# Performance work log

Hardware: AMD Instinct MI355X
Metric: run time of the kernel (lower is better)

The kernel has to match this reference:

```python
import math
import jax, jax.numpy as jnp
import numpy as np

N_HEAD = 32
HEAD_DIM = 64
ROTARY_DIM = 32
ROTARY_BASE = 10000.0


def _rope(u, cos, sin):
    # u: [B, S, H, head_dim]; cos/sin: [S, ROTARY_DIM//2]
    u_rot = u[..., :ROTARY_DIM].astype(jnp.float32)
    u1, u2 = jnp.split(u_rot, 2, axis=-1)          # [B,S,H,rot/2] each
    c = cos[None, :, None, :]
    s = sin[None, :, None, :]
    r = jnp.concatenate([u1 * c - u2 * s, u1 * s + u2 * c], axis=-1).astype(u.dtype)
    return jnp.concatenate([r, u[..., ROTARY_DIM:]], axis=-1)


def setup_inputs() -> dict:
    key = jax.random.key(0)
    ks = jax.random.split(key, 5)
    B, S, D = 2, 2048, 2048
    std = 1.0 / math.sqrt(D)
    x = jax.random.normal(ks[0], (B, S, D), dtype=jnp.float32)
    Wqkv = jax.random.normal(ks[1], (D, 3 * D), dtype=jnp.float32) * std
    b_qkv = jax.random.normal(ks[2], (3 * D,), dtype=jnp.float32) * 0.01
    Wout = jax.random.normal(ks[3], (D, D), dtype=jnp.float32) * std
    b_out = jax.random.normal(ks[4], (D,), dtype=jnp.float32) * 0.01
    return {"x": x, "Wqkv": Wqkv, "b_qkv": b_qkv, "Wout": Wout, "b_out": b_out}


def reference(x, Wqkv, b_qkv, Wout, b_out):
    B, S, D = x.shape
    H, hd = N_HEAD, HEAD_DIM
    # QKV projection -> [B, S, 3, H, hd]
    qkv = (x @ Wqkv + b_qkv).reshape(B, S, 3, H, hd)
    # Rotary cos/sin cache (fp32 position indices, as in the module)
    inv_freq = 1.0 / (ROTARY_BASE ** (jnp.arange(0, ROTARY_DIM, 2, dtype=jnp.float32) / ROTARY_DIM))
    t = jnp.arange(S, dtype=jnp.float32)
    freqs = jnp.outer(t, inv_freq)                 # [S, ROTARY_DIM//2]
    cos, sin = jnp.cos(freqs), jnp.sin(freqs)
    q = _rope(qkv[:, :, 0], cos, sin)
    k = _rope(qkv[:, :, 1], cos, sin)
    v = qkv[:, :, 2]
    scale = 1.0 / math.sqrt(hd)
    scores = jnp.einsum('bthd,bshd->bhts', q, k * scale)   # [B,H,S,S]
    rows = jnp.arange(S)[:, None]
    cols = jnp.arange(S)[None, :]
    causal_mask = cols > rows                      # seqlen_k == seqlen_q here
    scores = jnp.where(causal_mask[None, None], jnp.asarray(-10000.0, scores.dtype), scores)
    attn = jax.nn.softmax(scores, axis=-1)         # dropout p=0.0
    out = jnp.einsum('bhts,bshd->bthd', attn, v).reshape(B, S, D)
    return out @ Wout + b_out
```

## Files before the change

kernel.cpp:

```cpp
#include <hip/hip_runtime.h>
#include <stdint.h>
#include <math.h>

#define DEV static __device__ __forceinline__

typedef __attribute__((ext_vector_type(8))) short bf16x8;
typedef __attribute__((ext_vector_type(4))) float f32x4;
typedef __attribute__((ext_vector_type(8))) unsigned short u16x8;
typedef __attribute__((ext_vector_type(4))) unsigned short u16x4;
typedef __attribute__((ext_vector_type(2))) unsigned int u32x2;

enum { B_ = 2, S_ = 2048, D_ = 2048, H_ = 32, HD_ = 64, N3_ = 6144, M_ = 4096 };

DEV unsigned short f2bf(float f) {
  unsigned u = __float_as_uint(f);
  u += 0x7FFFu + ((u >> 16) & 1u);
  return (unsigned short)(u >> 16);
}
DEV float bf2f(unsigned short s) { return __uint_as_float(((unsigned)s) << 16); }

DEV void load16(const void* g, void* l) {
  __builtin_amdgcn_global_load_lds((const __attribute__((address_space(1))) void*)g,
                                   (__attribute__((address_space(3))) void*)l,
                                   16, 0, 0);
}

DEV f32x4 mfma16(bf16x8 a, bf16x8 b, f32x4 c) {
  return __builtin_amdgcn_mfma_f32_16x16x32_bf16(a, b, c, 0, 0, 0);
}

__global__ __launch_bounds__(256) void cvt_bf16(const float* __restrict__ in,
                                                unsigned short* __restrict__ out, int n) {
  int i = blockIdx.x * 256 + threadIdx.x;
  if (i * 8 >= n) return;
  const float4* in4 = (const float4*)in;
  float4 a = in4[i * 2 + 0];
  float4 b = in4[i * 2 + 1];
  u16x8 o;
  o[0] = f2bf(a.x); o[1] = f2bf(a.y); o[2] = f2bf(a.z); o[3] = f2bf(a.w);
  o[4] = f2bf(b.x); o[5] = f2bf(b.y); o[6] = f2bf(b.z); o[7] = f2bf(b.w);
  *(u16x8*)(out + (size_t)i * 8) = o;
}

__global__ __launch_bounds__(256) void transpose_bf16(const float* __restrict__ W,
                                                      unsigned short* __restrict__ Wt,
                                                      int Kg, int Ng) {
  __shared__ float tile[32][33];
  const int tn = blockIdx.x, tk = blockIdx.y;
  const int t = threadIdx.x;
  const int r = t >> 3, c4 = (t & 7) * 4;
  float4 v = *(const float4*)(W + (size_t)(tk * 32 + r) * Ng + tn * 32 + c4);
  tile[r][c4 + 0] = v.x; tile[r][c4 + 1] = v.y;
  tile[r][c4 + 2] = v.z; tile[r][c4 + 3] = v.w;
  __syncthreads();
  u16x4 o;
  o[0] = f2bf(tile[c4 + 0][r]);
  o[1] = f2bf(tile[c4 + 1][r]);
  o[2] = f2bf(tile[c4 + 2][r]);
  o[3] = f2bf(tile[c4 + 3][r]);
  *(u16x4*)(Wt + (size_t)(tn * 32 + r) * Kg + tk * 32 + c4) = o;
}

template <int MODE>
__global__ __launch_bounds__(512, 2) void gemm256(const unsigned short* __restrict__ A,
                                                  const unsigned short* __restrict__ BT,
                                                  const float* __restrict__ bias,
                                                  void* __restrict__ Cout,
                                                  int Mg, int Ng, int Kg) {
  __shared__ __align__(16) char lds[131072];
  const int tid = threadIdx.x;
  const int lane = tid & 63, w = tid >> 6;
  const int g = (lane >> 4) & 3, l16 = lane & 15;
  const int wm = w >> 2, wn = w & 3;

  const int wg = (blockIdx.x & 7) * (gridDim.x >> 3) + (blockIdx.x >> 3);
  const int nTM = Mg >> 8;
  const int tm = wg % nTM, tn = wg / nTM;
  const int rb = tm * 256, cb = tn * 256;
  const int NT = Kg >> 6;

  const int offA = (wm * 128 + l16) * 128;
  const int offB = 32768 + (wn * 64 + l16) * 128;
  const int su0 = ((0 + g) ^ (l16 & 7)) * 16;
  const int su1 = ((4 + g) ^ (l16 & 7)) * 16;

  const unsigned short* sA[4]; const unsigned short* sB[4];
  int dA[4], dB[4];
#pragma unroll
  for (int c = 0; c < 4; ++c) {
    int Uc = c * 512 + tid, row = Uc >> 3, u = (Uc & 7) ^ (row & 7);
    sA[c] = A + (size_t)(rb + row) * Kg + u * 8;
    sB[c] = BT + (size_t)(cb + row) * Kg + u * 8;
    dA[c] = Uc * 16; dB[c] = 32768 + Uc * 16;
  }

  auto STAGE = [&](int t) {
    char* _b = (char*)lds + ((t & 1) << 16);
#pragma unroll
    for (int c = 0; c < 4; ++c) {
      load16(sA[c] + (size_t)t * 64, _b + dA[c]);
      load16(sB[c] + (size_t)t * 64, _b + dB[c]);
    }
  };

  STAGE(0); STAGE(1);
  asm volatile("s_waitcnt vmcnt(8)" ::: "memory");
  __builtin_amdgcn_s_barrier();

  f32x4 acc[8][4] = {};

  for (int t = 0; t < NT; ++t) {
    const char* bs = (const char*)lds + ((t & 1) << 16);
    bf16x8 a[4][2], b[4][2];
#pragma unroll
    for (int mf = 0; mf < 4; ++mf) {
      a[mf][0] = *(const bf16x8*)(bs + offA + mf * 2048 + su0);
      a[mf][1] = *(const bf16x8*)(bs + offA + mf * 2048 + su1);
    }
#pragma unroll
    for (int nf = 0; nf < 4; ++nf) {
      b[nf][0] = *(const bf16x8*)(bs + offB + nf * 2048 + su0);
      b[nf][1] = *(const bf16x8*)(bs + offB + nf * 2048 + su1);
    }
#pragma unroll
    for (int mf = 0; mf < 4; ++mf)
#pragma unroll
      for (int nf = 0; nf < 4; ++nf)
#pragma unroll
        for (int kh = 0; kh < 2; ++kh)
          acc[mf][nf] = mfma16(a[mf][kh], b[nf][kh], acc[mf][nf]);
#pragma unroll
    for (int mf = 0; mf < 4; ++mf) {
      a[mf][0] = *(const bf16x8*)(bs + offA + (mf + 4) * 2048 + su0);
      a[mf][1] = *(const bf16x8*)(bs + offA + (mf + 4) * 2048 + su1);
    }
#pragma unroll
    for (int mf = 0; mf < 4; ++mf)
#pragma unroll
      for (int nf = 0; nf < 4; ++nf)
#pragma unroll
        for (int kh = 0; kh < 2; ++kh)
          acc[mf + 4][nf] = mfma16(a[mf][kh], b[nf][kh], acc[mf + 4][nf]);

    asm volatile("s_waitcnt lgkmcnt(0)" ::: "memory");
    __builtin_amdgcn_s_barrier();
    if (t + 2 < NT) {
      STAGE(t + 2);
      asm volatile("s_waitcnt vmcnt(8)" ::: "memory");
    } else {
      asm volatile("s_waitcnt vmcnt(0)" ::: "memory");
    }
    __builtin_amdgcn_s_barrier();
  }

  const int crow0 = rb + wm * 128 + g * 4;
  const int ccol0 = cb + wn * 64 + l16;
  float bv[4];
#pragma unroll
  for (int nf = 0; nf < 4; ++nf) bv[nf] = bias[ccol0 + nf * 16];

  if (MODE == 1) {
    unsigned short* O = (unsigned short*)Cout;
    const bool dorot = (cb + wn * 64) < 4096;
    const float inv = exp2f(-(float)l16 * 0.83048202372184056f);
#pragma unroll
    for (int mf = 0; mf < 8; ++mf)
#pragma unroll
      for (int r = 0; r < 4; ++r) {
        int row = crow0 + mf * 16 + r;
        float v0 = acc[mf][0][r] + bv[0];
        float v1 = acc[mf][1][r] + bv[1];
        float v2 = acc[mf][2][r] + bv[2];
        float v3 = acc[mf][3][r] + bv[3];
        if (dorot) {
          float sn, cs;
          sincosf((float)(row & (S_ - 1)) * inv, &sn, &cs);
          float t0 = v0 * cs - v1 * sn;
          v1 = v0 * sn + v1 * cs;
          v0 = t0;
        }
        unsigned short* p = O + (size_t)row * Ng + ccol0;
        p[0] = f2bf(v0); p[16] = f2bf(v1); p[32] = f2bf(v2); p[48] = f2bf(v3);
      }
  } else {
    float* O = (float*)Cout;
#pragma unroll
    for (int mf = 0; mf < 8; ++mf)
#pragma unroll
      for (int r = 0; r < 4; ++r) {
        int row = crow0 + mf * 16 + r;
        float* p = O + (size_t)row * Ng + ccol0;
        p[0] = acc[mf][0][r] + bv[0];
        p[16] = acc[mf][1][r] + bv[1];
        p[32] = acc[mf][2][r] + bv[2];
        p[48] = acc[mf][3][r] + bv[3];
      }
  }
}

DEV int xsw(int row) { return (row ^ (row >> 2)) & 3; }

template <int OUT_BF16>
__global__ __launch_bounds__(256) void gemm_bt(const unsigned short* __restrict__ A,
                                               const unsigned short* __restrict__ BT,
                                               const float* __restrict__ bias,
                                               void* __restrict__ Cout,
                                               int Mg, int Ng, int Kg) {
  __shared__ __align__(16) unsigned short lA[128 * 32];
  __shared__ __align__(16) unsigned short lB[128 * 32];
  const int tid = threadIdx.x;
  const int lane = tid & 63, wv = tid >> 6;
  const int g = lane >> 4, l16 = lane & 15;
  const int wr = wv >> 1, wc = wv & 1;
  const int rb = blockIdx.x * 128, cb = blockIdx.y * 128;

  f32x4 acc[4][4] = {};

  for (int k0 = 0; k0 < Kg; k0 += 32) {
    __syncthreads();
#pragma unroll
    for (int c = 0; c < 2; ++c) {
      int p = c * 256 + tid;
      int row = p >> 2;
      int k8l = (p & 3) ^ xsw(row);
      load16(A + (size_t)(rb + row) * Kg + k0 + 8 * k8l, (char*)lA + p * 16);
      load16(BT + (size_t)(cb + row) * Kg + k0 + 8 * k8l, (char*)lB + p * 16);
    }
    __syncthreads();
    bf16x8 af[4], bfr[4];
#pragma unroll
    for (int m = 0; m < 4; ++m) {
      int row = wr * 64 + m * 16 + l16;
      af[m] = *(const bf16x8*)((const char*)lA + (size_t)(row * 4 + (g ^ xsw(row))) * 16);
    }
#pragma unroll
    for (int n = 0; n < 4; ++n) {
      int row = wc * 64 + n * 16 + l16;
      bfr[n] = *(const bf16x8*)((const char*)lB + (size_t)(row * 4 + (g ^ xsw(row))) * 16);
    }
#pragma unroll
    for (int m = 0; m < 4; ++m)
#pragma unroll
      for (int n = 0; n < 4; ++n)
        acc[m][n] = mfma16(af[m], bfr[n], acc[m][n]);
  }

#pragma unroll
  for (int m = 0; m < 4; ++m)
#pragma unroll
    for (int n = 0; n < 4; ++n)
#pragma unroll
      for (int r = 0; r < 4; ++r) {
        int row = rb + wr * 64 + m * 16 + g * 4 + r;
        int col = cb + wc * 64 + n * 16 + l16;
        float v = acc[m][n][r] + bias[col];
        if (OUT_BF16)
          ((unsigned short*)Cout)[(size_t)row * Ng + col] = f2bf(v);
        else
          ((float*)Cout)[(size_t)row * Ng + col] = v;
      }
}

__global__ __launch_bounds__(256) void vtrans(const unsigned short* __restrict__ qkv,
                                              unsigned short* __restrict__ vt) {
  __shared__ unsigned short tile[64][72];
  const int s0 = blockIdx.x * 64;
  const int bh = blockIdx.y;
  const int b = bh >> 5, h = bh & 31;
  const int t = threadIdx.x;
#pragma unroll
  for (int c = 0; c < 2; ++c) {
    int sl = (c * 256 + t) >> 3, d8 = t & 7;
    u16x8 v = *(const u16x8*)(qkv + (size_t)(b * S_ + s0 + sl) * N3_ + 4096 + h * 64 + d8 * 8);
    *(u16x8*)(&tile[sl][d8 * 8]) = v;
  }
  __syncthreads();
#pragma unroll
  for (int c = 0; c < 2; ++c) {
    int dl = (c * 256 + t) >> 3, s8 = t & 7;
    u16x8 o;
#pragma unroll
    for (int j = 0; j < 8; ++j) o[j] = tile[s8 * 8 + j][dl];
    *(u16x8*)(vt + (size_t)(bh * 64 + dl) * S_ + s0 + s8 * 8) = o;
  }
}

DEV void stage_kv(const unsigned short* __restrict__ qkv,
                  const unsigned short* __restrict__ vt,
                  unsigned char* lds, int bS, int bh64, int hoff, int kvb, int buf, int tid) {
#pragma unroll
  for (int c = 0; c < 2; ++c) {
    int p = c * 256 + tid;
    int row = p >> 3, k8 = (p & 7) ^ (row & 7);
    load16(qkv + (size_t)(bS + kvb + row) * N3_ + 2048 + hoff + 8 * k8,
           lds + buf * 8192 + p * 16);
    load16(vt + (size_t)(bh64 + row) * S_ + kvb + 8 * k8,
           lds + 16384 + buf * 8192 + p * 16);
  }
}

__global__ __launch_bounds__(256, 3) void attn_kernel(const unsigned short* __restrict__ qkv,
                                                      const unsigned short* __restrict__ vt,
                                                      unsigned short* __restrict__ ao) {
  __shared__ __align__(16) unsigned char lds[49152];
  const int tid = threadIdx.x;
  const int lane = tid & 63, wv = tid >> 6;
  const int g = lane >> 4, l16 = lane & 15;
  const int bid = blockIdx.x;
  const int qi = 15 - (bid >> 6);
  const int t6 = bid & 63;
  const int bh = ((t6 & 7) << 3) | (t6 >> 3);
  const int b = bh >> 5, h = bh & 31;
  const int qbase = qi * 128;
  const int srow0 = qbase + wv * 32;
  const int bS = b * S_, bh64 = bh * 64, hoff = h * 64;

  bf16x8 qf[2][2];
#pragma unroll
  for (int m = 0; m < 2; ++m)
#pragma unroll
    for (int kt = 0; kt < 2; ++kt)
      qf[m][kt] = *(const bf16x8*)(qkv + (size_t)(bS + srow0 + m * 16 + l16) * N3_ +
                                   hoff + kt * 32 + g * 8);

  float mrun[2] = {-INFINITY, -INFINITY}, lrun[2] = {0.f, 0.f};
  f32x4 o[2][4] = {};
  unsigned char* pw = lds + 32768 + wv * 4096;

  const int nkv = (qbase + 128) >> 6;
  stage_kv(qkv, vt, lds, bS, bh64, hoff, 0, 0, tid);
  __syncthreads();

  for (int kb = 0; kb < nkv; ++kb) {
    const int cur = kb & 1;
    if (kb + 1 < nkv) stage_kv(qkv, vt, lds, bS, bh64, hoff, (kb + 1) << 6, cur ^ 1, tid);
    const int kvb = kb << 6;
    if (kvb <= srow0 + 31) {
      const unsigned char* kbuf = lds + cur * 8192;
      const unsigned char* vbuf = lds + 16384 + cur * 8192;

      f32x4 sc[2][4];
#pragma unroll
      for (int n = 0; n < 4; ++n) {
        int row = n * 16 + l16;
        bf16x8 kf0 = *(const bf16x8*)(kbuf + (row * 8 + ((g + 0) ^ (row & 7))) * 16);
        bf16x8 kf1 = *(const bf16x8*)(kbuf + (row * 8 + ((g + 4) ^ (row & 7))) * 16);
#pragma unroll
        for (int m = 0; m < 2; ++m) {
          f32x4 z = {};
          z = mfma16(kf0, qf[m][0], z);
          z = mfma16(kf1, qf[m][1], z);
          sc[m][n] = z;
        }
      }

      const bool boundary = (kvb + 63 > srow0);
#pragma unroll
      for (int m = 0; m < 2; ++m) {
        const int qrow = srow0 + m * 16 + l16;
        if (boundary) {
#pragma unroll
          for (int n = 0; n < 4; ++n)
#pragma unroll
            for (int r = 0; r < 4; ++r) {
              int k = kvb + n * 16 + g * 4 + r;
              if (k > qrow) sc[m][n][r] = -INFINITY;
            }
        }
        float mx = fmaxf(fmaxf(sc[m][0][0], sc[m][0][1]), fmaxf(sc[m][0][2], sc[m][0][3]));
#pragma unroll
        for (int n = 1; n < 4; ++n)
          mx = fmaxf(mx, fmaxf(fmaxf(sc[m][n][0], sc[m][n][1]), fmaxf(sc[m][n][2], sc[m][n][3])));
        mx = fmaxf(mx, __shfl_xor(mx, 16));
        mx = fmaxf(mx, __shfl_xor(mx, 32));
        float pm = mx * 0.125f;
        if (!__all(pm <= mrun[m] + 8.0f)) {
          float mn = fmaxf(mrun[m], pm);
          float al = exp2f((mrun[m] - mn) * 1.44269504f);
          mrun[m] = mn; lrun[m] *= al;
#pragma unroll
          for (int d = 0; d < 4; ++d) o[m][d] *= al;
        }
        const float mt = mrun[m] * 1.44269504f;
        float p[4][4]; float rs = 0.f;
#pragma unroll
        for (int n = 0; n < 4; ++n)
#pragma unroll
          for (int r = 0; r < 4; ++r) {
            p[n][r] = exp2f(fmaf(sc[m][n][r], 0.18033688011112042f, -mt));
            rs += p[n][r];
          }
        rs += __shfl_xor(rs, 16);
        rs += __shfl_xor(rs, 32);
        lrun[m] += rs;
#pragma unroll
        for (int n = 0; n < 4; ++n) {
          unsigned lo, hi;
          asm("v_cvt_pk_bf16_f32 %0, %1, %2" : "=v"(lo) : "v"(p[n][0]), "v"(p[n][1]));
          asm("v_cvt_pk_bf16_f32 %0, %1, %2" : "=v"(hi) : "v"(p[n][2]), "v"(p[n][3]));
          int su = (n * 4 + g) ^ ((l16 & 7) << 1);
          u32x2 wq; wq[0] = lo; wq[1] = hi;
          *(u32x2*)(pw + ((m * 16 + l16) * 16 + su) * 8) = wq;
        }
      }

      bf16x8 pf[2][2];
#pragma unroll
      for (int m = 0; m < 2; ++m)
#pragma unroll
        for (int kt = 0; kt < 2; ++kt) {
          int su = (kt * 8 + g * 2) ^ ((l16 & 7) << 1);
          pf[m][kt] = *(const bf16x8*)(pw + ((m * 16 + l16) * 16 + su) * 8);
        }
#pragma unroll
      for (int dblk = 0; dblk < 4; ++dblk) {
        int row = dblk * 16 + l16;
        bf16x8 vf0 = *(const bf16x8*)(vbuf + (row * 8 + ((g + 0) ^ (row & 7))) * 16);
        bf16x8 vf1 = *(const bf16x8*)(vbuf + (row * 8 + ((g + 4) ^ (row & 7))) * 16);
#pragma unroll
        for (int m = 0; m < 2; ++m) {
          o[m][dblk] = mfma16(vf0, pf[m][0], o[m][dblk]);
          o[m][dblk] = mfma16(vf1, pf[m][1], o[m][dblk]);
        }
      }
    }
    __syncthreads();
  }

#pragma unroll
  for (int m = 0; m < 2; ++m) {
    float inv = 1.0f / lrun[m];
    int q = srow0 + m * 16 + l16;
#pragma unroll
    for (int dblk = 0; dblk < 4; ++dblk) {
      u16x4 ov;
#pragma unroll
      for (int r = 0; r < 4; ++r) ov[r] = f2bf(o[m][dblk][r] * inv);
      *(u16x4*)(ao + (size_t)(bS + q) * D_ + hoff + dblk * 16 + g * 4) = ov;
    }
  }
}

extern "C" void kernel_launch(void* const* d_in, const int* in_sizes, int n_in,
                              void* d_out, int out_size, void* d_ws, size_t ws_size,
                              hipStream_t stream) {
  const float* x = (const float*)d_in[0];
  const float* Wqkv = (const float*)d_in[1];
  const float* bqkv = (const float*)d_in[2];
  const float* Wout = (const float*)d_in[3];
  const float* bout = (const float*)d_in[4];
  float* out = (float*)d_out;

  char* ws = (char*)d_ws;
  unsigned short* Xb = (unsigned short*)(ws + 0);
  unsigned short* Wqkvt = (unsigned short*)(ws + 16777216);
  unsigned short* Woutt = (unsigned short*)(ws + 41943040);
  unsigned short* QKVb = (unsigned short*)(ws + 50331648);
  unsigned short* Vt = (unsigned short*)(ws + 100663296);
  unsigned short* AO = Xb;

  cvt_bf16<<<4096, 256, 0, stream>>>(x, Xb, M_ * D_);
  transpose_bf16<<<dim3(192, 64), 256, 0, stream>>>(Wqkv, Wqkvt, 2048, 6144);
  transpose_bf16<<<dim3(64, 64), 256, 0, stream>>>(Wout, Woutt, 2048, 2048);
  gemm256<1><<<384, 512, 0, stream>>>(Xb, Wqkvt, bqkv, QKVb, M_, N3_, D_);
  vtrans<<<dim3(32, 64), 256, 0, stream>>>(QKVb, Vt);
  attn_kernel<<<1024, 256, 0, stream>>>(QKVb, Vt, AO);
  gemm_bt<0><<<dim3(32, 16), 256, 0, stream>>>(AO, Woutt, bout, out, M_, D_, D_);
}
```

Before: 287.1 us.

## Split GEMM main loop into ping-pong phases with setprio and finer LDS fragment loads

```diff
diff --git a/kernel.cpp b/kernel.cpp
--- a/kernel.cpp
+++ b/kernel.cpp
@@ -84,22 +84,22 @@
   const int su0 = ((0 + g) ^ (l16 & 7)) * 16;
   const int su1 = ((4 + g) ^ (l16 & 7)) * 16;
 
-  const unsigned short* sA[4]; const unsigned short* sB[4];
-  int dA[4], dB[4];
-#pragma unroll
-  for (int c = 0; c < 4; ++c) {
-    int Uc = c * 512 + tid, row = Uc >> 3, u = (Uc & 7) ^ (row & 7);
-    sA[c] = A + (size_t)(rb + row) * Kg + u * 8;
-    sB[c] = BT + (size_t)(cb + row) * Kg + u * 8;
-    dA[c] = Uc * 16; dB[c] = 32768 + Uc * 16;
-  }
+  const int r0 = tid >> 3;
+  const int u8e = ((tid & 7) ^ (r0 & 7)) * 8;
+  const unsigned short* sA = A + (size_t)(rb + r0) * Kg + u8e;
+  const unsigned short* sB = BT + (size_t)(cb + r0) * Kg + u8e;
+  const size_t cstep = (size_t)Kg << 6;
+  char* const dA0 = (char*)lds + tid * 16;
 
   auto STAGE = [&](int t) {
-    char* _b = (char*)lds + ((t & 1) << 16);
+    char* db = dA0 + ((t & 1) << 16);
+    const size_t to = (size_t)t << 5;
+    (void)to;
+    const size_t toff = (size_t)t * 64;
 #pragma unroll
     for (int c = 0; c < 4; ++c) {
-      load16(sA[c] + (size_t)t * 64, _b + dA[c]);
-      load16(sB[c] + (size_t)t * 64, _b + dB[c]);
+      load16(sA + c * cstep + toff, db + c * 8192);
+      load16(sB + c * cstep + toff, db + 32768 + c * 8192);
     }
   };
 
@@ -111,38 +111,52 @@
 
   for (int t = 0; t < NT; ++t) {
     const char* bs = (const char*)lds + ((t & 1) << 16);
-    bf16x8 a[4][2], b[4][2];
+    bf16x8 a0[4][2], a1[4][2], b01[2][2], b23[2][2];
 #pragma unroll
     for (int mf = 0; mf < 4; ++mf) {
-      a[mf][0] = *(const bf16x8*)(bs + offA + mf * 2048 + su0);
-      a[mf][1] = *(const bf16x8*)(bs + offA + mf * 2048 + su1);
-    }
-#pragma unroll
-    for (int nf = 0; nf < 4; ++nf) {
-      b[nf][0] = *(const bf16x8*)(bs + offB + nf * 2048 + su0);
-      b[nf][1] = *(const bf16x8*)(bs + offB + nf * 2048 + su1);
-    }
+      a0[mf][0] = *(const bf16x8*)(bs + offA + mf * 2048 + su0);
+      a0[mf][1] = *(const bf16x8*)(bs + offA + mf * 2048 + su1);
+    }
+#pragma unroll
+    for (int nf = 0; nf < 2; ++nf) {
+      b01[nf][0] = *(const bf16x8*)(bs + offB + nf * 2048 + su0);
+      b01[nf][1] = *(const bf16x8*)(bs + offB + nf * 2048 + su1);
+    }
+    asm volatile("s_waitcnt lgkmcnt(8)" ::: "memory");
+    __builtin_amdgcn_s_barrier();
+    asm volatile("s_waitcnt lgkmcnt(0)" ::: "memory");
+    __builtin_amdgcn_s_setprio(1);
 #pragma unroll
     for (int mf = 0; mf < 4; ++mf)
 #pragma unroll
-      for (int nf = 0; nf < 4; ++nf)
+      for (int nf = 0; nf < 2; ++nf)
 #pragma unroll
         for (int kh = 0; kh < 2; ++kh)
-          acc[mf][nf] = mfma16(a[mf][kh], b[nf][kh], acc[mf][nf]);
+          acc[mf][nf] = mfma16(a0[mf][kh], b01[nf][kh], acc[mf][nf]);
+    __builtin_amdgcn_s_setprio(0);
+    __builtin_amdgcn_s_barrier();
 #pragma unroll
     for (int mf = 0; mf < 4; ++mf) {
-      a[mf][0] = *(const bf16x8*)(bs + offA + (mf + 4) * 2048 + su0);
-      a[mf][1] = *(const bf16x8*)(bs + offA + (mf + 4) * 2048 + su1);
-    }
+      a1[mf][0] = *(const bf16x8*)(bs + offA + (mf + 4) * 2048 + su0);
+      a1[mf][1] = *(const bf16x8*)(bs + offA + (mf + 4) * 2048 + su1);
+    }
+#pragma unroll
+    for (int nf = 0; nf < 2; ++nf) {
+      b23[nf][0] = *(const bf16x8*)(bs + offB + (nf + 2) * 2048 + su0);
+      b23[nf][1] = *(const bf16x8*)(bs + offB + (nf + 2) * 2048 + su1);
+    }
+    asm volatile("s_waitcnt lgkmcnt(8)" ::: "memory");
+    __builtin_amdgcn_s_barrier();
+    asm volatile("s_waitcnt lgkmcnt(0)" ::: "memory");
+    __builtin_amdgcn_s_setprio(1);
 #pragma unroll
     for (int mf = 0; mf < 4; ++mf)
 #pragma unroll
-      for (int nf = 0; nf < 4; ++nf)
+      for (int nf = 0; nf < 2; ++nf)
 #pragma unroll
         for (int kh = 0; kh < 2; ++kh)
-          acc[mf + 4][nf] = mfma16(a[mf][kh], b[nf][kh], acc[mf + 4][nf]);
-
-    asm volatile("s_waitcnt lgkmcnt(0)" ::: "memory");
+          acc[mf][nf + 2] = mfma16(a0[mf][kh], b23[nf][kh], acc[mf][nf + 2]);
+    __builtin_amdgcn_s_setprio(0);
     __builtin_amdgcn_s_barrier();
     if (t + 2 < NT) {
       STAGE(t + 2);
@@ -150,6 +164,23 @@
     } else {
       asm volatile("s_waitcnt vmcnt(0)" ::: "memory");
     }
+    __builtin_amdgcn_s_barrier();
+    __builtin_amdgcn_s_setprio(1);
+#pragma unroll
+    for (int mf = 0; mf < 4; ++mf)
+#pragma unroll
+      for (int nf = 0; nf < 2; ++nf)
+#pragma unroll
+        for (int kh = 0; kh < 2; ++kh)
+          acc[mf + 4][nf] = mfma16(a1[mf][kh], b01[nf][kh], acc[mf + 4][nf]);
+#pragma unroll
+    for (int mf = 0; mf < 4; ++mf)
+#pragma unroll
+      for (int nf = 0; nf < 2; ++nf)
+#pragma unroll
+        for (int kh = 0; kh < 2; ++kh)
+          acc[mf + 4][nf + 2] = mfma16(a1[mf][kh], b23[nf][kh], acc[mf + 4][nf + 2]);
+    __builtin_amdgcn_s_setprio(0);
     __builtin_amdgcn_s_barrier();
   }
 
```

Measured after the change: 302.0 us. 1.05x slower.
